# Optimization experiments

Measured on AMD Instinct MI355X. Metric: run time of the kernel, lower is better.

Reference implementation:

```python
import jax, jax.numpy as jnp
import numpy as np

DIM = 512
HEADS = 8
HEAD_DIM = DIM // HEADS
B, N = 4, 8192


def setup_inputs() -> dict:
    key = jax.random.key(0)
    k1, k2, k3, k4 = jax.random.split(key, 4)
    x = jax.random.normal(k1, (B, N, DIM), dtype=jnp.float32)
    # torch Linear weight is [out, in]; store transposed [in, out] for x @ W
    Wqkv = jax.random.normal(k2, (DIM, 3 * DIM), dtype=jnp.float32) * (DIM ** -0.5)
    Wout = jax.random.normal(k3, (DIM, DIM), dtype=jnp.float32) * (DIM ** -0.5)
    bout = jax.random.normal(k4, (DIM,), dtype=jnp.float32) * 0.01
    return {"x": x, "Wqkv": Wqkv, "Wout": Wout, "bout": bout}


def reference(x, Wqkv, Wout, bout):
    b, n, d = x.shape
    h, hd = HEADS, HEAD_DIM
    qkv = x @ Wqkv  # [b, n, 3d]
    q, k, v = jnp.split(qkv, 3, axis=-1)
    # [b, n, d] -> [b, h, n, hd]
    def to_heads(t):
        return t.reshape(b, n, h, hd).transpose(0, 2, 1, 3)
    q, k, v = to_heads(q), to_heads(k), to_heads(v)
    q = jax.nn.elu(q) + 1.0
    k = jax.nn.elu(k) + 1.0
    kv = jnp.einsum('bhnd,bhne->bhde', k, v)          # [b,h,hd,hd]
    z = 1.0 / (jnp.einsum('bhnd,bhd->bhn', q, k.sum(axis=2)) + 1e-6)
    out = jnp.einsum('bhnd,bhde->bhne', q, kv) * z[..., None]
    out = out.transpose(0, 2, 1, 3).reshape(b, n, d)
    # dropout in eval mode is identity
    return out @ Wout + bout
```

## Files before the change

### kernel.cpp

```cpp
#include <hip/hip_runtime.h>

typedef unsigned short u16;
typedef __bf16 bf16x8 __attribute__((ext_vector_type(8)));
typedef float f32x4 __attribute__((ext_vector_type(4)));

#define DEV static __device__ __forceinline__

DEV float bf2f(u16 u) { unsigned x = ((unsigned)u) << 16; return __builtin_bit_cast(float, x); }
DEV u16 f2bf(float f) {
  unsigned u = __builtin_bit_cast(unsigned, f);
  u += 0x7FFFu + ((u >> 16) & 1u);
  return (u16)(u >> 16);
}
DEV int swz(int b) { return b ^ ((((b >> 7) & 7)) << 4); }

#define GLD_LDS16(gp, lp)                                                    \
  __builtin_amdgcn_global_load_lds(                                          \
      (__attribute__((address_space(1))) void*)(void*)(gp),                  \
      (__attribute__((address_space(3))) void*)(lp), 16, 0, 0)

#define BAR() __builtin_amdgcn_s_barrier()
#define WAIT_LGKM0()                                                         \
  { asm volatile("s_waitcnt lgkmcnt(0)" ::: "memory");                       \
    __builtin_amdgcn_sched_barrier(0); }
#define WAIT_VM(n) asm volatile("s_waitcnt vmcnt(" #n ")" ::: "memory")

__global__ __launch_bounds__(256) void convert_bf16_kernel(
    const float* __restrict__ in, u16* __restrict__ out) {
  const size_t i = (size_t)blockIdx.x * 256 + threadIdx.x;
  const float4* p = (const float4*)in + 2 * i;
  float4 a = p[0], b = p[1];
  unsigned w0 = (unsigned)f2bf(a.x) | ((unsigned)f2bf(a.y) << 16);
  unsigned w1 = (unsigned)f2bf(a.z) | ((unsigned)f2bf(a.w) << 16);
  unsigned w2 = (unsigned)f2bf(b.x) | ((unsigned)f2bf(b.y) << 16);
  unsigned w3 = (unsigned)f2bf(b.z) | ((unsigned)f2bf(b.w) << 16);
  ((uint4*)out)[i] = make_uint4(w0, w1, w2, w3);
}

__global__ void transpose_bf16(const float* __restrict__ W, u16* __restrict__ Wt,
                               int K, int Ncols) {
  __shared__ float t[32][33];
  const int tx = threadIdx.x & 31, ty = threadIdx.x >> 5;
  const int n0 = blockIdx.x * 32, k0 = blockIdx.y * 32;
#pragma unroll
  for (int i = 0; i < 4; ++i)
    t[ty + i * 8][tx] = W[(size_t)(k0 + ty + i * 8) * Ncols + n0 + tx];
  __syncthreads();
#pragma unroll
  for (int i = 0; i < 4; ++i)
    Wt[(size_t)(n0 + ty + i * 8) * K + k0 + tx] = f2bf(t[tx][ty + i * 8]);
}

template <int MODE>
__global__ __launch_bounds__(512, 2) void gemm8_kernel(
    const u16* __restrict__ A, const u16* __restrict__ Bt,
    u16* __restrict__ qb, u16* __restrict__ kb, u16* __restrict__ vb,
    float* __restrict__ Cf, const float* __restrict__ bias) {
  constexpr int NX = (MODE == 0) ? 6 : 2;
  constexpr int K = 512;
  __shared__ __align__(16) u16 As[2][2][8192];
  __shared__ __align__(16) u16 Bs[2][2][8192];

  const int tid = threadIdx.x;
  const int lane = tid & 63;
  const int wid = tid >> 6;
  const int wr = wid >> 2;
  const int wcn = wid & 3;

  const int nwg = gridDim.x;
  const int pb = blockIdx.x;
  const int logical = (pb & 7) * (nwg >> 3) + (pb >> 3);
  const int rowBase = (logical / NX) * 256;
  const int colBase = (logical % NX) * 256;

  int soff[2], od[2];
#pragma unroll
  for (int i = 0; i < 2; ++i) {
    int o = (wid * 2 + i) * 1024 + lane * 16;
    int a = o ^ (((o >> 7) & 7) << 4);
    soff[i] = (a >> 7) * K + ((a & 127) >> 1);
    od[i] = (wid * 2 + i) * 512;
  }
  const u16* Abase = A + (size_t)rowBase * K;
  const u16* Bbase = Bt + (size_t)colBase * K;

#define STAGE_A(tau, h)                                                      \
  { const u16* g = Abase + (size_t)(h)*128 * K + (tau)*64;                   \
    _Pragma("unroll") for (int i = 0; i < 2; ++i)                            \
        GLD_LDS16(g + soff[i], &As[(tau)&1][h][od[i]]); }
#define STAGE_B(tau, h)                                                      \
  { const u16* g = Bbase + (size_t)(h)*128 * K + (tau)*64;                   \
    _Pragma("unroll") for (int i = 0; i < 2; ++i)                            \
        GLD_LDS16(g + soff[i], &Bs[(tau)&1][h][od[i]]); }

  const int sx = (lane & 7) << 4;
  int rb[2];
#pragma unroll
  for (int ks = 0; ks < 2; ++ks)
    rb[ks] = ((lane & 15) * 128 + ks * 64 + (lane >> 4) * 16) ^ sx;
  const char* Ahalf[2] = {(const char*)&As[0][wr][0], (const char*)&As[1][wr][0]};
  const char* Bhalf[2] = {(const char*)&Bs[0][wcn >> 1][0], (const char*)&Bs[1][wcn >> 1][0]};

  bf16x8 aA[4][2], bB0[2][2], bB1[2][2];
  f32x4 acc[8][4];
  f32x4 zv = {0.f, 0.f, 0.f, 0.f};
#pragma unroll
  for (int m = 0; m < 8; ++m)
#pragma unroll
    for (int n = 0; n < 4; ++n) acc[m][n] = zv;

#define LDA_FRAGS(par, mh)                                                   \
  _Pragma("unroll") for (int m = 0; m < 4; ++m)                              \
      _Pragma("unroll") for (int ks = 0; ks < 2; ++ks)                       \
          aA[m][ks] = *(const bf16x8*)(Ahalf[par] + (mh)*8192 + m * 2048 + rb[ks]);
#define LDB_FRAGS(par, nh, dst)                                              \
  _Pragma("unroll") for (int n = 0; n < 2; ++n)                              \
      _Pragma("unroll") for (int ks = 0; ks < 2; ++ks)                       \
          dst[n][ks] = *(const bf16x8*)(Bhalf[par] + (wcn & 1) * 8192 +      \
                                        (nh)*4096 + n * 2048 + rb[ks]);
#define MFMA_QUAD(mh, nh, bsrc)                                              \
  __builtin_amdgcn_s_setprio(1);                                             \
  _Pragma("unroll") for (int m = 0; m < 4; ++m)                              \
      _Pragma("unroll") for (int n = 0; n < 2; ++n)                          \
          _Pragma("unroll") for (int ks = 0; ks < 2; ++ks)                   \
              acc[(mh)*4 + m][(nh)*2 + n] =                                  \
                  __builtin_amdgcn_mfma_f32_16x16x32_bf16(                   \
                      aA[m][ks], bsrc[n][ks], acc[(mh)*4 + m][(nh)*2 + n],   \
                      0, 0, 0);                                              \
  __builtin_amdgcn_s_setprio(0);

  STAGE_A(0, 0); STAGE_A(0, 1); STAGE_B(0, 0); STAGE_B(0, 1);
  STAGE_B(1, 0); STAGE_A(1, 0);
  WAIT_VM(4);
  BAR();

  for (int t = 0; t < 6; t += 2) {
    LDA_FRAGS(0, 0); LDB_FRAGS(0, 0, bB0);
    STAGE_B(t + 1, 1);
    BAR(); WAIT_LGKM0();
    MFMA_QUAD(0, 0, bB0);
    BAR();
    LDB_FRAGS(0, 1, bB1);
    STAGE_A(t + 1, 1);
    BAR(); WAIT_LGKM0();
    MFMA_QUAD(0, 1, bB1);
    BAR();
    LDA_FRAGS(0, 1);
    STAGE_B(t + 2, 0);
    BAR(); WAIT_LGKM0();
    MFMA_QUAD(1, 1, bB1);
    BAR();
    STAGE_A(t + 2, 0);
    BAR(); WAIT_LGKM0();
    MFMA_QUAD(1, 0, bB0);
    WAIT_VM(4);
    BAR();
    LDA_FRAGS(1, 0); LDB_FRAGS(1, 0, bB0);
    STAGE_A(t + 2, 1);
    BAR(); WAIT_LGKM0();
    MFMA_QUAD(0, 0, bB0);
    BAR();
    LDB_FRAGS(1, 1, bB1);
    STAGE_B(t + 2, 1);
    BAR(); WAIT_LGKM0();
    MFMA_QUAD(0, 1, bB1);
    BAR();
    LDA_FRAGS(1, 1);
    STAGE_B(t + 3, 0);
    BAR(); WAIT_LGKM0();
    MFMA_QUAD(1, 1, bB1);
    BAR();
    STAGE_A(t + 3, 0);
    BAR(); WAIT_LGKM0();
    MFMA_QUAD(1, 0, bB0);
    WAIT_VM(4);
    BAR();
  }

  LDA_FRAGS(0, 0); LDB_FRAGS(0, 0, bB0);
  STAGE_B(7, 1);
  BAR(); WAIT_LGKM0();
  MFMA_QUAD(0, 0, bB0);
  BAR();
  LDB_FRAGS(0, 1, bB1);
  STAGE_A(7, 1);
  BAR(); WAIT_LGKM0();
  MFMA_QUAD(0, 1, bB1);
  BAR();
  LDA_FRAGS(0, 1);
  BAR(); WAIT_LGKM0();
  MFMA_QUAD(1, 1, bB1);
  BAR();
  BAR(); WAIT_LGKM0();
  MFMA_QUAD(1, 0, bB0);
  WAIT_VM(0);
  BAR();
  LDA_FRAGS(1, 0); LDB_FRAGS(1, 0, bB0);
  BAR(); WAIT_LGKM0();
  MFMA_QUAD(0, 0, bB0);
  BAR();
  LDB_FRAGS(1, 1, bB1);
  BAR(); WAIT_LGKM0();
  MFMA_QUAD(0, 1, bB1);
  BAR();
  LDA_FRAGS(1, 1);
  BAR(); WAIT_LGKM0();
  MFMA_QUAD(1, 1, bB1);
  BAR();
  BAR(); WAIT_LGKM0();
  MFMA_QUAD(1, 0, bB0);

  if (MODE == 0) {
    u16* dst = (colBase < 512) ? qb : (colBase < 1024) ? kb : vb;
    const int cb2 = colBase & 511;
    const bool doelu = (colBase < 1024);
    const int rbBase = (rowBase >> 4) + wr * 8;
    const int cbBase = (cb2 >> 4) + wcn * 4;
#pragma unroll
    for (int mi = 0; mi < 8; ++mi) {
#pragma unroll
      for (int ni = 0; ni < 4; ++ni) {
        float v[4];
#pragma unroll
        for (int r = 0; r < 4; ++r) {
          float t2 = acc[mi][ni][r];
          v[r] = doelu ? ((t2 > 0.f) ? t2 + 1.f : __expf(t2)) : t2;
        }
        unsigned lo = (unsigned)f2bf(v[0]) | ((unsigned)f2bf(v[1]) << 16);
        unsigned hi = (unsigned)f2bf(v[2]) | ((unsigned)f2bf(v[3]) << 16);
        size_t base = (((size_t)(rbBase + mi) * 32 + (cbBase + ni)) * 64 + lane) * 4;
        *(uint2*)(dst + base) = make_uint2(lo, hi);
      }
    }
  } else {
#pragma unroll
    for (int mi = 0; mi < 8; ++mi) {
#pragma unroll
      for (int ni = 0; ni < 4; ++ni) {
        const int col = colBase + wcn * 64 + ni * 16 + (lane & 15);
#pragma unroll
        for (int r = 0; r < 4; ++r) {
          const int row = rowBase + wr * 128 + mi * 16 + (lane >> 4) * 4 + r;
          Cf[(size_t)row * 512 + col] = acc[mi][ni][r] + bias[col];
        }
      }
    }
  }
#undef STAGE_A
#undef STAGE_B
#undef LDA_FRAGS
#undef LDB_FRAGS
#undef MFMA_QUAD
}

__global__ __launch_bounds__(256, 2) void kv_partial_mfma(
    const u16* __restrict__ kb, const u16* __restrict__ vb,
    float* __restrict__ part) {
  __shared__ __align__(16) char lds[81920];
  const int tid = threadIdx.x, lane = tid & 63, wid = tid >> 6;
  const int chunk = blockIdx.x;
  const int bh = blockIdx.y;
  const int b = bh >> 3, h = bh & 7;
  const int hcb = h * 4;

  char* kTc = lds + wid * 16384;
  char* vTc = kTc + 8192;
  const int rb0 = b * 512 + chunk * 64 + wid * 16;

  uint4 kreg[8], vreg[8];

#define KV_LOAD(it)                                                          \
  _Pragma("unroll") for (int q = 0; q < 8; ++q) {                            \
    int u = q * 64 + lane;                                                   \
    int fid = u >> 5, w = u & 31;                                            \
    int rbl = fid >> 2, cbi = fid & 3;                                       \
    size_t fb = ((size_t)(rb0 + (it)*4 + rbl) * 32 + hcb + cbi) * 32 + w;    \
    kreg[q] = ((const uint4*)kb)[fb];                                        \
    vreg[q] = ((const uint4*)vb)[fb];                                        \
  }

#define KV_WRITE()                                                           \
  _Pragma("unroll") for (int q = 0; q < 8; ++q) {                            \
    int u = q * 64 + lane;                                                   \
    int fid = u >> 5, w = u & 31;                                            \
    int rbl = fid >> 2, cbi = fid & 3;                                       \
    int l0 = 2 * w;                                                          \
    int d0 = cbi * 16 + (l0 & 15);                                           \
    int n0 = rbl * 16 + (l0 >> 4) * 4;                                       \
    int a0 = swz(d0 * 128 + n0 * 2);                                         \
    int a1 = swz((d0 + 1) * 128 + n0 * 2);                                   \
    *(uint2*)(kTc + a0) = make_uint2(kreg[q].x, kreg[q].y);                  \
    *(uint2*)(kTc + a1) = make_uint2(kreg[q].z, kreg[q].w);                  \
    *(uint2*)(vTc + a0) = make_uint2(vreg[q].x, vreg[q].y);                  \
    *(uint2*)(vTc + a1) = make_uint2(vreg[q].z, vreg[q].w);                  \
  }

  const uint4 onesu = make_uint4(0x3F803F80u, 0x3F803F80u, 0x3F803F80u, 0x3F803F80u);
  const bf16x8 ones = __builtin_bit_cast(bf16x8, onesu);

  f32x4 zv = {0.f, 0.f, 0.f, 0.f};
  f32x4 acc[4][5];
#pragma unroll
  for (int mb = 0; mb < 4; ++mb)
#pragma unroll
    for (int eb = 0; eb < 5; ++eb) acc[mb][eb] = zv;

  KV_LOAD(0);
#pragma unroll
  for (int it = 0; it < 4; ++it) {
    WAIT_VM(0);
    KV_WRITE();
    if (it < 3) KV_LOAD(it + 1);
    WAIT_LGKM0();
#pragma unroll
    for (int ks = 0; ks < 2; ++ks) {
      bf16x8 afr[4], bvf[4];
#pragma unroll
      for (int mb = 0; mb < 4; ++mb)
        afr[mb] = *(const bf16x8*)(kTc + swz((mb * 16 + (lane & 15)) * 128 +
                                             (ks * 32 + (lane >> 4) * 8) * 2));
#pragma unroll
      for (int eb = 0; eb < 4; ++eb)
        bvf[eb] = *(const bf16x8*)(vTc + swz((eb * 16 + (lane & 15)) * 128 +
                                             (ks * 32 + (lane >> 4) * 8) * 2));
      WAIT_LGKM0();
#pragma unroll
      for (int mb = 0; mb < 4; ++mb) {
#pragma unroll
        for (int eb = 0; eb < 4; ++eb)
          acc[mb][eb] = __builtin_amdgcn_mfma_f32_16x16x32_bf16(
              afr[mb], bvf[eb], acc[mb][eb], 0, 0, 0);
        acc[mb][4] = __builtin_amdgcn_mfma_f32_16x16x32_bf16(
            afr[mb], ones, acc[mb][4], 0, 0, 0);
      }
    }
  }

  __syncthreads();
  float* red = (float*)lds;
#pragma unroll
  for (int mb = 0; mb < 4; ++mb)
#pragma unroll
    for (int eb = 0; eb < 5; ++eb)
      ((f32x4*)red)[wid * 1280 + (mb * 5 + eb) * 64 + lane] = acc[mb][eb];
  __syncthreads();

  float* pp = part + ((size_t)bh * 8 + chunk) * 5120;
  const int lane_s = tid >> 2, r = tid & 3;
#pragma unroll
  for (int fi = 0; fi < 20; ++fi) {
    float s = red[fi * 256 + tid] + red[5120 + fi * 256 + tid] +
              red[10240 + fi * 256 + tid] + red[15360 + fi * 256 + tid];
    const int mb = fi / 5, eb = fi % 5;
    const int d = mb * 16 + (lane_s >> 4) * 4 + r;
    if (eb < 4) {
      pp[d * 80 + eb * 16 + (lane_s & 15)] = s;
    } else if ((lane_s & 15) == 0) {
      pp[d * 80 + 64] = s;
    }
  }
#undef KV_LOAD
#undef KV_WRITE
}

__global__ void kv_reduce_kernel(const float* __restrict__ part,
                                 float* __restrict__ kv_ext) {
  const int idx = blockIdx.x * 256 + threadIdx.x;
  const int bh = idx / 5120;
  const int de = idx % 5120;
  const int e = de % 80;
  float s = 0.f;
  if (e <= 64) {
    for (int c = 0; c < 8; ++c) s += part[((size_t)bh * 8 + c) * 5120 + de];
  }
  kv_ext[idx] = s;
}

__global__ __launch_bounds__(256, 2) void attn_kernel(
    const u16* __restrict__ qb, const float* __restrict__ kv_ext,
    u16* __restrict__ attn) {
  __shared__ __align__(16) float kvs[64 * 80];
  __shared__ __align__(16) u16 qs[4][64 * 64];
  const int tid = threadIdx.x, lane = tid & 63, wid = tid >> 6;
  const int nchunk = blockIdx.x, bh = blockIdx.y;
  const int b = bh >> 3, h = bh & 7;

#pragma unroll
  for (int i = 0; i < 20; ++i)
    kvs[i * 256 + tid] = kv_ext[(size_t)bh * 5120 + i * 256 + tid];
  __syncthreads();

  bf16x8 bfr[5][2];
#pragma unroll
  for (int eb = 0; eb < 5; ++eb)
#pragma unroll
    for (int ksi = 0; ksi < 2; ++ksi) {
      unsigned pw[4];
#pragma unroll
      for (int jj = 0; jj < 4; ++jj) {
        int d0 = ksi * 32 + (lane >> 4) * 8 + 2 * jj;
        int e = eb * 16 + (lane & 15);
        unsigned lo = f2bf(kvs[d0 * 80 + e]);
        unsigned hi = f2bf(kvs[(d0 + 1) * 80 + e]);
        pw[jj] = lo | (hi << 16);
      }
      uint4 u = make_uint4(pw[0], pw[1], pw[2], pw[3]);
      bfr[eb][ksi] = __builtin_bit_cast(bf16x8, u);
    }

  const size_t row0 = (size_t)b * 8192 + (size_t)nchunk * 256 + wid * 64;
  const int rbQ = (int)(row0 >> 4);
  const int hcbQ = h * 4;
  char* qsw = (char*)&qs[wid][0];
#pragma unroll
  for (int it = 0; it < 8; ++it) {
    int flat = it * 64 + lane;
    int frag = flat >> 5, w = flat & 31;
    int rb_i = frag >> 2, cb_i = frag & 3;
    size_t src = (((size_t)(rbQ + rb_i) * 32 + hcbQ + cb_i) * 64 + w * 2) * 4;
    uint4 q4 = *(const uint4*)(qb + src);
    int l0 = w * 2;
    int row = rb_i * 16 + ((l0 >> 4) << 2);
    int col = cb_i * 16 + (l0 & 15);
    int bb = row * 128 + col * 2;
    *(unsigned*)(qsw + swz(bb)) = (q4.x & 0xFFFF) | ((q4.z & 0xFFFF) << 16);
    *(unsigned*)(qsw + swz(bb + 128)) = (q4.x >> 16) | (q4.z & 0xFFFF0000u);
    *(unsigned*)(qsw + swz(bb + 256)) = (q4.y & 0xFFFF) | ((q4.w & 0xFFFF) << 16);
    *(unsigned*)(qsw + swz(bb + 384)) = (q4.y >> 16) | (q4.w & 0xFFFF0000u);
  }
  WAIT_LGKM0();

  f32x4 zv = {0.f, 0.f, 0.f, 0.f};
  f32x4 acc[4][5];
#pragma unroll
  for (int m = 0; m < 4; ++m)
#pragma unroll
    for (int eb = 0; eb < 5; ++eb) acc[m][eb] = zv;

#pragma unroll
  for (int m = 0; m < 4; ++m)
#pragma unroll
    for (int ksi = 0; ksi < 2; ++ksi) {
      int bb = (m * 16 + (lane & 15)) * 128 + (ksi * 32 + (lane >> 4) * 8) * 2;
      bf16x8 af = *(const bf16x8*)(qsw + swz(bb));
#pragma unroll
      for (int eb = 0; eb < 5; ++eb)
        acc[m][eb] = __builtin_amdgcn_mfma_f32_16x16x32_bf16(af, bfr[eb][ksi], acc[m][eb], 0, 0, 0);
    }

#pragma unroll
  for (int m = 0; m < 4; ++m) {
#pragma unroll
    for (int r = 0; r < 4; ++r) {
      float den = __shfl(acc[m][4][r], lane & ~15, 64);
      float zr = 1.f / (den + 1e-6f);
      int row = m * 16 + (lane >> 4) * 4 + r;
#pragma unroll
      for (int eb = 0; eb < 4; ++eb) {
        int col = eb * 16 + (lane & 15);
        *(u16*)(qsw + swz(row * 128 + col * 2)) = f2bf(acc[m][eb][r] * zr);
      }
    }
  }
  WAIT_LGKM0();
#pragma unroll
  for (int jt = 0; jt < 8; ++jt) {
    int flat = jt * 64 + lane;
    int row = flat >> 3, w = flat & 7;
    uint4 val = *(const uint4*)(qsw + swz(row * 128 + w * 16));
    *(uint4*)(attn + (row0 + row) * 512 + h * 64 + w * 8) = val;
  }
}

extern "C" void kernel_launch(void* const* d_in, const int* in_sizes, int n_in,
                              void* d_out, int out_size, void* d_ws, size_t ws_size,
                              hipStream_t stream) {
  const float* x = (const float*)d_in[0];
  const float* Wqkv = (const float*)d_in[1];
  const float* Wout = (const float*)d_in[2];
  const float* bout = (const float*)d_in[3];
  float* out = (float*)d_out;

  char* ws = (char*)d_ws;
  u16* qb = (u16*)ws;        ws += (size_t)32768 * 512 * 2;
  u16* kb = (u16*)ws;        ws += (size_t)32768 * 512 * 2;
  u16* vb = (u16*)ws;        ws += (size_t)32768 * 512 * 2;
  u16* wqkv_t = (u16*)ws;    ws += (size_t)1536 * 512 * 2;
  u16* wout_t = (u16*)ws;    ws += (size_t)512 * 512 * 2;
  float* kv_ext = (float*)ws; ws += (size_t)32 * 64 * 80 * 4;
  float* part = (float*)ws;   ws += (size_t)32 * 8 * 64 * 80 * 4;

  u16* xb = (u16*)d_out;

  convert_bf16_kernel<<<8192, 256, 0, stream>>>(x, xb);
  transpose_bf16<<<dim3(1536 / 32, 512 / 32), 256, 0, stream>>>(Wqkv, wqkv_t, 512, 1536);
  transpose_bf16<<<dim3(512 / 32, 512 / 32), 256, 0, stream>>>(Wout, wout_t, 512, 512);
  gemm8_kernel<0><<<768, 512, 0, stream>>>(xb, wqkv_t, qb, kb, vb, nullptr, nullptr);
  kv_partial_mfma<<<dim3(8, 32), 256, 0, stream>>>(kb, vb, part);
  kv_reduce_kernel<<<640, 256, 0, stream>>>(part, kv_ext);
  attn_kernel<<<dim3(32, 32), 256, 0, stream>>>(qb, kv_ext, vb);
  gemm8_kernel<1><<<256, 512, 0, stream>>>(vb, wout_t, nullptr, nullptr, nullptr, out, bout);
}
```

Before: 144.5 us.

## Make QKV GEMM persistent over three output tiles per workgroup

The QKV projection GEMM now launches 256 workgroups, each covering three consecutive 256x256 output tiles rather than one. The K-loop runs across all three tiles, so staging of the next tile's A/B slices overlaps the current tile's MFMAs, and the per-tile epilogue runs inside the loop before the accumulators are reset. This removes the per-tile pipeline prologue and drain and the launch of 768 separate workgroups. The tile order changes so consecutive tiles step along rows within a column panel. On a 256-CU part this gives one workgroup per CU, which may reduce latency hiding and leaves the mid-loop epilogue exposed while the prefetched loads are in flight.

```diff
diff --git a/kernel.cpp b/kernel.cpp
--- a/kernel.cpp
+++ b/kernel.cpp
@@ -56,7 +56,8 @@
     const u16* __restrict__ A, const u16* __restrict__ Bt,
     u16* __restrict__ qb, u16* __restrict__ kb, u16* __restrict__ vb,
     float* __restrict__ Cf, const float* __restrict__ bias) {
-  constexpr int NX = (MODE == 0) ? 6 : 2;
+  constexpr int PANELS = (MODE == 0) ? 3 : 1;
+  constexpr int NT = 8 * PANELS;
   constexpr int K = 512;
   __shared__ __align__(16) u16 As[2][2][8192];
   __shared__ __align__(16) u16 Bs[2][2][8192];
@@ -70,8 +71,7 @@
   const int nwg = gridDim.x;
   const int pb = blockIdx.x;
   const int logical = (pb & 7) * (nwg >> 3) + (pb >> 3);
-  const int rowBase = (logical / NX) * 256;
-  const int colBase = (logical % NX) * 256;
+  const int T0 = logical * PANELS;
 
   int soff[2], od[2];
 #pragma unroll
@@ -81,17 +81,17 @@
     soff[i] = (a >> 7) * K + ((a & 127) >> 1);
     od[i] = (wid * 2 + i) * 512;
   }
-  const u16* Abase = A + (size_t)rowBase * K;
-  const u16* Bbase = Bt + (size_t)colBase * K;
-
-#define STAGE_A(tau, h)                                                      \
-  { const u16* g = Abase + (size_t)(h)*128 * K + (tau)*64;                   \
+
+#define STAGE_A(s, h)                                                        \
+  { int _T = T0 + ((s) >> 3);                                                \
+    const u16* g = A + (size_t)((_T & 127) * 256 + (h)*128) * K + ((s)&7) * 64; \
     _Pragma("unroll") for (int i = 0; i < 2; ++i)                            \
-        GLD_LDS16(g + soff[i], &As[(tau)&1][h][od[i]]); }
-#define STAGE_B(tau, h)                                                      \
-  { const u16* g = Bbase + (size_t)(h)*128 * K + (tau)*64;                   \
+        GLD_LDS16(g + soff[i], &As[(s)&1][h][od[i]]); }
+#define STAGE_B(s, h)                                                        \
+  { int _T = T0 + ((s) >> 3);                                                \
+    const u16* g = Bt + (size_t)((_T >> 7) * 256 + (h)*128) * K + ((s)&7) * 64; \
     _Pragma("unroll") for (int i = 0; i < 2; ++i)                            \
-        GLD_LDS16(g + soff[i], &Bs[(tau)&1][h][od[i]]); }
+        GLD_LDS16(g + soff[i], &Bs[(s)&1][h][od[i]]); }
 
   const int sx = (lane & 7) << 4;
   int rb[2];
@@ -129,12 +129,51 @@
                       0, 0, 0);                                              \
   __builtin_amdgcn_s_setprio(0);
 
+#define EPILOGUE(pp)                                                         \
+  { const int _Te = T0 + (pp);                                               \
+    const int rowB = (_Te & 127) * 256, colB = (_Te >> 7) * 256;             \
+    if (MODE == 0) {                                                         \
+      u16* dst = (colB < 512) ? qb : (colB < 1024) ? kb : vb;                \
+      const int cb2 = colB & 511;                                            \
+      const bool doelu = (colB < 1024);                                      \
+      const int rbB = (rowB >> 4) + wr * 8;                                  \
+      const int cbB = (cb2 >> 4) + wcn * 4;                                  \
+      _Pragma("unroll") for (int mi = 0; mi < 8; ++mi) {                     \
+        _Pragma("unroll") for (int ni = 0; ni < 4; ++ni) {                   \
+          float v[4];                                                        \
+          _Pragma("unroll") for (int r = 0; r < 4; ++r) {                    \
+            float t2 = acc[mi][ni][r];                                       \
+            v[r] = doelu ? ((t2 > 0.f) ? t2 + 1.f : __expf(t2)) : t2;        \
+          }                                                                  \
+          unsigned lo = (unsigned)f2bf(v[0]) | ((unsigned)f2bf(v[1]) << 16); \
+          unsigned hi = (unsigned)f2bf(v[2]) | ((unsigned)f2bf(v[3]) << 16); \
+          size_t base = (((size_t)(rbB + mi) * 32 + (cbB + ni)) * 64 + lane) * 4; \
+          *(uint2*)(dst + base) = make_uint2(lo, hi);                        \
+        }                                                                    \
+      }                                                                      \
+    } else {                                                                 \
+      _Pragma("unroll") for (int mi = 0; mi < 8; ++mi) {                     \
+        _Pragma("unroll") for (int ni = 0; ni < 4; ++ni) {                   \
+          const int col = colB + wcn * 64 + ni * 16 + (lane & 15);           \
+          _Pragma("unroll") for (int r = 0; r < 4; ++r) {                    \
+            const int row = rowB + wr * 128 + mi * 16 + (lane >> 4) * 4 + r; \
+            Cf[(size_t)row * 512 + col] = acc[mi][ni][r] + bias[col];        \
+          }                                                                  \
+        }                                                                    \
+      }                                                                      \
+    }                                                                        \
+  }
+#define ZERO_ACC()                                                           \
+  _Pragma("unroll") for (int m = 0; m < 8; ++m)                              \
+      _Pragma("unroll") for (int n = 0; n < 4; ++n) acc[m][n] = zv;
+
   STAGE_A(0, 0); STAGE_A(0, 1); STAGE_B(0, 0); STAGE_B(0, 1);
   STAGE_B(1, 0); STAGE_A(1, 0);
   WAIT_VM(4);
   BAR();
 
-  for (int t = 0; t < 6; t += 2) {
+#pragma unroll 1
+  for (int t = 0; t < NT - 2; t += 2) {
     LDA_FRAGS(0, 0); LDB_FRAGS(0, 0, bB0);
     STAGE_B(t + 1, 1);
     BAR(); WAIT_LGKM0();
@@ -175,15 +214,19 @@
     MFMA_QUAD(1, 0, bB0);
     WAIT_VM(4);
     BAR();
+    if (PANELS > 1 && (t & 7) == 6) {
+      EPILOGUE((t + 1) >> 3);
+      ZERO_ACC();
+    }
   }
 
   LDA_FRAGS(0, 0); LDB_FRAGS(0, 0, bB0);
-  STAGE_B(7, 1);
+  STAGE_B(NT - 1, 1);
   BAR(); WAIT_LGKM0();
   MFMA_QUAD(0, 0, bB0);
   BAR();
   LDB_FRAGS(0, 1, bB1);
-  STAGE_A(7, 1);
+  STAGE_A(NT - 1, 1);
   BAR(); WAIT_LGKM0();
   MFMA_QUAD(0, 1, bB1);
   BAR();
@@ -210,47 +253,15 @@
   BAR(); WAIT_LGKM0();
   MFMA_QUAD(1, 0, bB0);
 
-  if (MODE == 0) {
-    u16* dst = (colBase < 512) ? qb : (colBase < 1024) ? kb : vb;
-    const int cb2 = colBase & 511;
-    const bool doelu = (colBase < 1024);
-    const int rbBase = (rowBase >> 4) + wr * 8;
-    const int cbBase = (cb2 >> 4) + wcn * 4;
-#pragma unroll
-    for (int mi = 0; mi < 8; ++mi) {
-#pragma unroll
-      for (int ni = 0; ni < 4; ++ni) {
-        float v[4];
-#pragma unroll
-        for (int r = 0; r < 4; ++r) {
-          float t2 = acc[mi][ni][r];
-          v[r] = doelu ? ((t2 > 0.f) ? t2 + 1.f : __expf(t2)) : t2;
-        }
-        unsigned lo = (unsigned)f2bf(v[0]) | ((unsigned)f2bf(v[1]) << 16);
-        unsigned hi = (unsigned)f2bf(v[2]) | ((unsigned)f2bf(v[3]) << 16);
-        size_t base = (((size_t)(rbBase + mi) * 32 + (cbBase + ni)) * 64 + lane) * 4;
-        *(uint2*)(dst + base) = make_uint2(lo, hi);
-      }
-    }
-  } else {
-#pragma unroll
-    for (int mi = 0; mi < 8; ++mi) {
-#pragma unroll
-      for (int ni = 0; ni < 4; ++ni) {
-        const int col = colBase + wcn * 64 + ni * 16 + (lane & 15);
-#pragma unroll
-        for (int r = 0; r < 4; ++r) {
-          const int row = rowBase + wr * 128 + mi * 16 + (lane >> 4) * 4 + r;
-          Cf[(size_t)row * 512 + col] = acc[mi][ni][r] + bias[col];
-        }
-      }
-    }
-  }
+  EPILOGUE(PANELS - 1);
+
 #undef STAGE_A
 #undef STAGE_B
 #undef LDA_FRAGS
 #undef LDB_FRAGS
 #undef MFMA_QUAD
+#undef EPILOGUE
+#undef ZERO_ACC
 }
 
 __global__ __launch_bounds__(256, 2) void kv_partial_mfma(
@@ -495,7 +506,7 @@
   convert_bf16_kernel<<<8192, 256, 0, stream>>>(x, xb);
   transpose_bf16<<<dim3(1536 / 32, 512 / 32), 256, 0, stream>>>(Wqkv, wqkv_t, 512, 1536);
   transpose_bf16<<<dim3(512 / 32, 512 / 32), 256, 0, stream>>>(Wout, wout_t, 512, 512);
-  gemm8_kernel<0><<<768, 512, 0, stream>>>(xb, wqkv_t, qb, kb, vb, nullptr, nullptr);
+  gemm8_kernel<0><<<256, 512, 0, stream>>>(xb, wqkv_t, qb, kb, vb, nullptr, nullptr);
   kv_partial_mfma<<<dim3(8, 32), 256, 0, stream>>>(kb, vb, part);
   kv_reduce_kernel<<<640, 256, 0, stream>>>(part, kv_ext);
   attn_kernel<<<dim3(32, 32), 256, 0, stream>>>(qb, kv_ext, vb);
```

Measured after the change: 156.5 us. 1.08x slower.

## Fuse fp32-to-bf16 conversion of x into QKV GEMM A-tile loading

Applied to the files above, without the earlier changes.

Removes the separate conversion kernel and has the QKV GEMM load fp32 x directly into registers. It then converts the values with v_cvt_pk_bf16_f32 and writes them to LDS, with the issue and write steps interleaved into the existing pipeline. This drops one kernel launch and the write and re-read of a bf16 copy of x. In exchange the GEMM reads twice the bytes for A, uses extra registers, and replaces direct global-to-LDS loads with register staging and new vmcnt waits.

```diff
diff --git a/kernel.cpp b/kernel.cpp
--- a/kernel.cpp
+++ b/kernel.cpp
@@ -12,6 +12,11 @@
   u += 0x7FFFu + ((u >> 16) & 1u);
   return (u16)(u >> 16);
 }
+DEV unsigned cvtpk(float lo, float hi) {
+  unsigned r;
+  asm("v_cvt_pk_bf16_f32 %0, %1, %2" : "=v"(r) : "v"(lo), "v"(hi));
+  return r;
+}
 DEV int swz(int b) { return b ^ ((((b >> 7) & 7)) << 4); }
 
 #define GLD_LDS16(gp, lp)                                                    \
@@ -25,18 +30,6 @@
     __builtin_amdgcn_sched_barrier(0); }
 #define WAIT_VM(n) asm volatile("s_waitcnt vmcnt(" #n ")" ::: "memory")
 
-__global__ __launch_bounds__(256) void convert_bf16_kernel(
-    const float* __restrict__ in, u16* __restrict__ out) {
-  const size_t i = (size_t)blockIdx.x * 256 + threadIdx.x;
-  const float4* p = (const float4*)in + 2 * i;
-  float4 a = p[0], b = p[1];
-  unsigned w0 = (unsigned)f2bf(a.x) | ((unsigned)f2bf(a.y) << 16);
-  unsigned w1 = (unsigned)f2bf(a.z) | ((unsigned)f2bf(a.w) << 16);
-  unsigned w2 = (unsigned)f2bf(b.x) | ((unsigned)f2bf(b.y) << 16);
-  unsigned w3 = (unsigned)f2bf(b.z) | ((unsigned)f2bf(b.w) << 16);
-  ((uint4*)out)[i] = make_uint4(w0, w1, w2, w3);
-}
-
 __global__ void transpose_bf16(const float* __restrict__ W, u16* __restrict__ Wt,
                                int K, int Ncols) {
   __shared__ float t[32][33];
@@ -53,7 +46,7 @@
 
 template <int MODE>
 __global__ __launch_bounds__(512, 2) void gemm8_kernel(
-    const u16* __restrict__ A, const u16* __restrict__ Bt,
+    const void* __restrict__ Av, const u16* __restrict__ Bt,
     u16* __restrict__ qb, u16* __restrict__ kb, u16* __restrict__ vb,
     float* __restrict__ Cf, const float* __restrict__ bias) {
   constexpr int NX = (MODE == 0) ? 6 : 2;
@@ -73,6 +66,9 @@
   const int rowBase = (logical / NX) * 256;
   const int colBase = (logical % NX) * 256;
 
+  const float* Axf = (const float*)Av;
+  const u16* Axb = (const u16*)Av;
+
   int soff[2], od[2];
 #pragma unroll
   for (int i = 0; i < 2; ++i) {
@@ -81,17 +77,32 @@
     soff[i] = (a >> 7) * K + ((a & 127) >> 1);
     od[i] = (wid * 2 + i) * 512;
   }
-  const u16* Abase = A + (size_t)rowBase * K;
+  const u16* Abase = Axb + (size_t)rowBase * K;
   const u16* Bbase = Bt + (size_t)colBase * K;
 
+#define STAGE_B(tau, h)                                                      \
+  { const u16* g = Bbase + (size_t)(h)*128 * K + (tau)*64;                   \
+    _Pragma("unroll") for (int i = 0; i < 2; ++i)                            \
+        GLD_LDS16(g + soff[i], &Bs[(tau)&1][h][od[i]]); }
 #define STAGE_A(tau, h)                                                      \
   { const u16* g = Abase + (size_t)(h)*128 * K + (tau)*64;                   \
     _Pragma("unroll") for (int i = 0; i < 2; ++i)                            \
         GLD_LDS16(g + soff[i], &As[(tau)&1][h][od[i]]); }
-#define STAGE_B(tau, h)                                                      \
-  { const u16* g = Bbase + (size_t)(h)*128 * K + (tau)*64;                   \
-    _Pragma("unroll") for (int i = 0; i < 2; ++i)                            \
-        GLD_LDS16(g + soff[i], &Bs[(tau)&1][h][od[i]]); }
+#define ISSUE_A(R, tau, h)                                                   \
+  { const float* g = Axf + (size_t)(rowBase + (h)*128) * K + (tau)*64;       \
+    _Pragma("unroll") for (int i = 0; i < 2; ++i) {                          \
+      R[2 * i] = *(const float4*)(g + soff[i]);                              \
+      R[2 * i + 1] = *(const float4*)(g + soff[i] + 4);                      \
+    } }
+#define WRITE_A(R, tau, h)                                                   \
+  { _Pragma("unroll") for (int i = 0; i < 2; ++i) {                          \
+      uint4 w;                                                               \
+      w.x = cvtpk(R[2 * i].x, R[2 * i].y);                                   \
+      w.y = cvtpk(R[2 * i].z, R[2 * i].w);                                   \
+      w.z = cvtpk(R[2 * i + 1].x, R[2 * i + 1].y);                           \
+      w.w = cvtpk(R[2 * i + 1].z, R[2 * i + 1].w);                           \
+      *(uint4*)&As[(tau)&1][h][od[i] + lane * 8] = w;                        \
+    } }
 
   const int sx = (lane & 7) << 4;
   int rb[2];
@@ -102,6 +113,7 @@
   const char* Bhalf[2] = {(const char*)&Bs[0][wcn >> 1][0], (const char*)&Bs[1][wcn >> 1][0]};
 
   bf16x8 aA[4][2], bB0[2][2], bB1[2][2];
+  float4 aR0[4], aR1[4];
   f32x4 acc[8][4];
   f32x4 zv = {0.f, 0.f, 0.f, 0.f};
 #pragma unroll
@@ -129,34 +141,52 @@
                       0, 0, 0);                                              \
   __builtin_amdgcn_s_setprio(0);
 
-  STAGE_A(0, 0); STAGE_A(0, 1); STAGE_B(0, 0); STAGE_B(0, 1);
-  STAGE_B(1, 0); STAGE_A(1, 0);
-  WAIT_VM(4);
-  BAR();
-
+  if constexpr (MODE == 0) {
+    ISSUE_A(aR0, 0, 0); ISSUE_A(aR1, 0, 1);
+    STAGE_B(0, 0); STAGE_B(0, 1);
+    WAIT_VM(8); WRITE_A(aR0, 0, 0);
+    WAIT_VM(4); WRITE_A(aR1, 0, 1);
+    ISSUE_A(aR0, 1, 0);
+    WAIT_VM(0); WRITE_A(aR0, 1, 0);
+    ISSUE_A(aR1, 1, 1); STAGE_B(1, 0);
+    WAIT_LGKM0();
+    BAR();
+  } else {
+    STAGE_A(0, 0); STAGE_A(0, 1); STAGE_B(0, 0); STAGE_B(0, 1);
+    STAGE_B(1, 0); STAGE_A(1, 0);
+    WAIT_VM(4);
+    BAR();
+  }
+
+#pragma unroll 1
   for (int t = 0; t < 6; t += 2) {
     LDA_FRAGS(0, 0); LDB_FRAGS(0, 0, bB0);
+    if constexpr (MODE == 0) { ISSUE_A(aR0, t + 2, 0); }
     STAGE_B(t + 1, 1);
     BAR(); WAIT_LGKM0();
     MFMA_QUAD(0, 0, bB0);
     BAR();
     LDB_FRAGS(0, 1, bB1);
-    STAGE_A(t + 1, 1);
+    if constexpr (MODE == 0) { WAIT_VM(8); WRITE_A(aR1, t + 1, 1); }
+    else { STAGE_A(t + 1, 1); }
     BAR(); WAIT_LGKM0();
     MFMA_QUAD(0, 1, bB1);
     BAR();
     LDA_FRAGS(0, 1);
+    if constexpr (MODE == 0) { ISSUE_A(aR1, t + 2, 1); }
     STAGE_B(t + 2, 0);
     BAR(); WAIT_LGKM0();
     MFMA_QUAD(1, 1, bB1);
     BAR();
-    STAGE_A(t + 2, 0);
+    if constexpr (MODE == 0) { WAIT_VM(6); WRITE_A(aR0, t + 2, 0); }
+    else { STAGE_A(t + 2, 0); }
     BAR(); WAIT_LGKM0();
     MFMA_QUAD(1, 0, bB0);
-    WAIT_VM(4);
+    if constexpr (MODE == 1) WAIT_VM(4);
     BAR();
     LDA_FRAGS(1, 0); LDB_FRAGS(1, 0, bB0);
-    STAGE_A(t + 2, 1);
+    if constexpr (MODE == 0) { ISSUE_A(aR0, t + 3, 0); WAIT_VM(6); WRITE_A(aR1, t + 2, 1); }
+    else { STAGE_A(t + 2, 1); }
     BAR(); WAIT_LGKM0();
     MFMA_QUAD(0, 0, bB0);
     BAR();
@@ -166,14 +196,16 @@
     MFMA_QUAD(0, 1, bB1);
     BAR();
     LDA_FRAGS(1, 1);
+    if constexpr (MODE == 0) { ISSUE_A(aR1, t + 3, 1); }
     STAGE_B(t + 3, 0);
     BAR(); WAIT_LGKM0();
     MFMA_QUAD(1, 1, bB1);
     BAR();
-    STAGE_A(t + 3, 0);
+    if constexpr (MODE == 0) { WAIT_VM(6); WRITE_A(aR0, t + 3, 0); }
+    else { STAGE_A(t + 3, 0); }
     BAR(); WAIT_LGKM0();
     MFMA_QUAD(1, 0, bB0);
-    WAIT_VM(4);
+    if constexpr (MODE == 1) WAIT_VM(4);
     BAR();
   }
 
@@ -183,7 +215,8 @@
   MFMA_QUAD(0, 0, bB0);
   BAR();
   LDB_FRAGS(0, 1, bB1);
-  STAGE_A(7, 1);
+  if constexpr (MODE == 0) { WAIT_VM(4); WRITE_A(aR1, 7, 1); }
+  else { STAGE_A(7, 1); }
   BAR(); WAIT_LGKM0();
   MFMA_QUAD(0, 1, bB1);
   BAR();
@@ -248,6 +281,8 @@
   }
 #undef STAGE_A
 #undef STAGE_B
+#undef ISSUE_A
+#undef WRITE_A
 #undef LDA_FRAGS
 #undef LDB_FRAGS
 #undef MFMA_QUAD
@@ -490,12 +525,9 @@
   float* kv_ext = (float*)ws; ws += (size_t)32 * 64 * 80 * 4;
   float* part = (float*)ws;   ws += (size_t)32 * 8 * 64 * 80 * 4;
 
-  u16* xb = (u16*)d_out;
-
-  convert_bf16_kernel<<<8192, 256, 0, stream>>>(x, xb);
   transpose_bf16<<<dim3(1536 / 32, 512 / 32), 256, 0, stream>>>(Wqkv, wqkv_t, 512, 1536);
   transpose_bf16<<<dim3(512 / 32, 512 / 32), 256, 0, stream>>>(Wout, wout_t, 512, 512);
-  gemm8_kernel<0><<<768, 512, 0, stream>>>(xb, wqkv_t, qb, kb, vb, nullptr, nullptr);
+  gemm8_kernel<0><<<768, 512, 0, stream>>>(x, wqkv_t, qb, kb, vb, nullptr, nullptr);
   kv_partial_mfma<<<dim3(8, 32), 256, 0, stream>>>(kb, vb, part);
   kv_reduce_kernel<<<640, 256, 0, stream>>>(part, kv_ext);
   attn_kernel<<<dim3(32, 32), 256, 0, stream>>>(qb, kv_ext, vb);
```

Measured after the change: 150.7 us. 1.04x slower.

## Fuse attention output computation into the output projection GEMM

Applied to the files above, without the earlier changes.

Removes the separate attn_kernel and generates the A operand of the output GEMM on the fly: each K-tile (one head) is computed from q fragments and the per-head kv matrix with MFMAs, normalized, and written directly into the swizzled LDS A buffer. The kv reduction now also pre-packs kv into bf16 MFMA fragment layout so the fused kernel can load it directly. This drops the global round-trip of the attention output and one launch. In exchange, the GEMM main loop has extra per-tile MFMA and LDS work plus more register pressure.

```diff
diff --git a/kernel.cpp b/kernel.cpp
--- a/kernel.cpp
+++ b/kernel.cpp
@@ -51,12 +51,10 @@
     Wt[(size_t)(n0 + ty + i * 8) * K + k0 + tx] = f2bf(t[tx][ty + i * 8]);
 }
 
-template <int MODE>
-__global__ __launch_bounds__(512, 2) void gemm8_kernel(
+__global__ __launch_bounds__(512, 2) void gemm_qkv_kernel(
     const u16* __restrict__ A, const u16* __restrict__ Bt,
-    u16* __restrict__ qb, u16* __restrict__ kb, u16* __restrict__ vb,
-    float* __restrict__ Cf, const float* __restrict__ bias) {
-  constexpr int NX = (MODE == 0) ? 6 : 2;
+    u16* __restrict__ qb, u16* __restrict__ kb, u16* __restrict__ vb) {
+  constexpr int NX = 6;
   constexpr int K = 512;
   __shared__ __align__(16) u16 As[2][2][8192];
   __shared__ __align__(16) u16 Bs[2][2][8192];
@@ -64,8 +62,7 @@
   const int tid = threadIdx.x;
   const int lane = tid & 63;
   const int wid = tid >> 6;
-  const int wr = wid >> 2;
-  const int wcn = wid & 3;
+  const int wr = wid >> 2, wcn = wid & 3;
 
   const int nwg = gridDim.x;
   const int pb = blockIdx.x;
@@ -210,7 +207,7 @@
   BAR(); WAIT_LGKM0();
   MFMA_QUAD(1, 0, bB0);
 
-  if (MODE == 0) {
+  {
     u16* dst = (colBase < 512) ? qb : (colBase < 1024) ? kb : vb;
     const int cb2 = colBase & 511;
     const bool doelu = (colBase < 1024);
@@ -230,19 +227,6 @@
         unsigned hi = (unsigned)f2bf(v[2]) | ((unsigned)f2bf(v[3]) << 16);
         size_t base = (((size_t)(rbBase + mi) * 32 + (cbBase + ni)) * 64 + lane) * 4;
         *(uint2*)(dst + base) = make_uint2(lo, hi);
-      }
-    }
-  } else {
-#pragma unroll
-    for (int mi = 0; mi < 8; ++mi) {
-#pragma unroll
-      for (int ni = 0; ni < 4; ++ni) {
-        const int col = colBase + wcn * 64 + ni * 16 + (lane & 15);
-#pragma unroll
-        for (int r = 0; r < 4; ++r) {
-          const int row = rowBase + wr * 128 + mi * 16 + (lane >> 4) * 4 + r;
-          Cf[(size_t)row * 512 + col] = acc[mi][ni][r] + bias[col];
-        }
       }
     }
   }
@@ -363,113 +347,212 @@
 #undef KV_WRITE
 }
 
-__global__ void kv_reduce_kernel(const float* __restrict__ part,
-                                 float* __restrict__ kv_ext) {
-  const int idx = blockIdx.x * 256 + threadIdx.x;
-  const int bh = idx / 5120;
-  const int de = idx % 5120;
-  const int e = de % 80;
-  float s = 0.f;
-  if (e <= 64) {
-    for (int c = 0; c < 8; ++c) s += part[((size_t)bh * 8 + c) * 5120 + de];
-  }
-  kv_ext[idx] = s;
-}
-
-__global__ __launch_bounds__(256, 2) void attn_kernel(
-    const u16* __restrict__ qb, const float* __restrict__ kv_ext,
-    u16* __restrict__ attn) {
-  __shared__ __align__(16) float kvs[64 * 80];
-  __shared__ __align__(16) u16 qs[4][64 * 64];
-  const int tid = threadIdx.x, lane = tid & 63, wid = tid >> 6;
-  const int nchunk = blockIdx.x, bh = blockIdx.y;
-  const int b = bh >> 3, h = bh & 7;
-
-#pragma unroll
-  for (int i = 0; i < 20; ++i)
-    kvs[i * 256 + tid] = kv_ext[(size_t)bh * 5120 + i * 256 + tid];
+__global__ __launch_bounds__(256) void kv_reduce_frag(
+    const float* __restrict__ part, uint4* __restrict__ kvf) {
+  __shared__ float kvs[5120];
+  const int tid = threadIdx.x;
+  const int bh = blockIdx.x;
+#pragma unroll
+  for (int i = 0; i < 20; ++i) {
+    int idx = i * 256 + tid;
+    float s = 0.f;
+    if (idx % 80 <= 64) {
+      for (int c = 0; c < 8; ++c) s += part[((size_t)bh * 8 + c) * 5120 + idx];
+    }
+    kvs[idx] = s;
+  }
   __syncthreads();
 
-  bf16x8 bfr[5][2];
-#pragma unroll
-  for (int eb = 0; eb < 5; ++eb)
-#pragma unroll
-    for (int ksi = 0; ksi < 2; ++ksi) {
+  const int lane = tid & 63, f = tid >> 6;
+#pragma unroll
+  for (int i = 0; i < 3; ++i) {
+    int combo = i * 4 + f;
+    if (combo < 10) {
+      int eb = combo >> 1, ks = combo & 1;
       unsigned pw[4];
 #pragma unroll
       for (int jj = 0; jj < 4; ++jj) {
-        int d0 = ksi * 32 + (lane >> 4) * 8 + 2 * jj;
+        int d0 = ks * 32 + (lane >> 4) * 8 + 2 * jj;
         int e = eb * 16 + (lane & 15);
         unsigned lo = f2bf(kvs[d0 * 80 + e]);
         unsigned hi = f2bf(kvs[(d0 + 1) * 80 + e]);
         pw[jj] = lo | (hi << 16);
       }
-      uint4 u = make_uint4(pw[0], pw[1], pw[2], pw[3]);
-      bfr[eb][ksi] = __builtin_bit_cast(bf16x8, u);
+      kvf[(size_t)bh * 640 + combo * 64 + lane] = make_uint4(pw[0], pw[1], pw[2], pw[3]);
     }
-
-  const size_t row0 = (size_t)b * 8192 + (size_t)nchunk * 256 + wid * 64;
-  const int rbQ = (int)(row0 >> 4);
-  const int hcbQ = h * 4;
-  char* qsw = (char*)&qs[wid][0];
-#pragma unroll
-  for (int it = 0; it < 8; ++it) {
-    int flat = it * 64 + lane;
-    int frag = flat >> 5, w = flat & 31;
-    int rb_i = frag >> 2, cb_i = frag & 3;
-    size_t src = (((size_t)(rbQ + rb_i) * 32 + hcbQ + cb_i) * 64 + w * 2) * 4;
-    uint4 q4 = *(const uint4*)(qb + src);
-    int l0 = w * 2;
-    int row = rb_i * 16 + ((l0 >> 4) << 2);
-    int col = cb_i * 16 + (l0 & 15);
-    int bb = row * 128 + col * 2;
-    *(unsigned*)(qsw + swz(bb)) = (q4.x & 0xFFFF) | ((q4.z & 0xFFFF) << 16);
-    *(unsigned*)(qsw + swz(bb + 128)) = (q4.x >> 16) | (q4.z & 0xFFFF0000u);
-    *(unsigned*)(qsw + swz(bb + 256)) = (q4.y & 0xFFFF) | ((q4.w & 0xFFFF) << 16);
-    *(unsigned*)(qsw + swz(bb + 384)) = (q4.y >> 16) | (q4.w & 0xFFFF0000u);
-  }
+  }
+}
+
+__global__ __launch_bounds__(512, 2) void gemm1f_kernel(
+    const u16* __restrict__ qb, const uint4* __restrict__ kvf,
+    const u16* __restrict__ Bt, float* __restrict__ Cf,
+    const float* __restrict__ bias) {
+  constexpr int K = 512;
+  __shared__ __align__(16) u16 As[2][2][8192];
+  __shared__ __align__(16) u16 Bs[2][2][8192];
+  __shared__ __align__(16) u16 qstage[8][1024];
+
+  const int tid = threadIdx.x, lane = tid & 63, wid = tid >> 6;
+  const int wr = wid >> 2, wcn = wid & 3;
+  const int nwg = gridDim.x, pb = blockIdx.x;
+  const int logical = (pb & 7) * (nwg >> 3) + (pb >> 3);
+  const int rowBase = (logical >> 1) * 256;
+  const int colBase = (logical & 1) * 256;
+  const int bIdx = rowBase >> 13;
+
+  int soff[2], od[2];
+#pragma unroll
+  for (int i = 0; i < 2; ++i) {
+    int o = (wid * 2 + i) * 1024 + lane * 16;
+    int a = o ^ (((o >> 7) & 7) << 4);
+    soff[i] = (a >> 7) * K + ((a & 127) >> 1);
+    od[i] = (wid * 2 + i) * 512;
+  }
+  const u16* Bbase = Bt + (size_t)colBase * K;
+
+#define STAGE_BF(tau)                                                        \
+  { _Pragma("unroll") for (int h = 0; h < 2; ++h) {                          \
+      const u16* g = Bbase + (size_t)h * 128 * K + (tau)*64;                 \
+      _Pragma("unroll") for (int i = 0; i < 2; ++i)                          \
+          GLD_LDS16(g + soff[i], &Bs[(tau)&1][h][od[i]]); } }
+
+  const int sx = (lane & 7) << 4;
+  int rb[2];
+#pragma unroll
+  for (int ks = 0; ks < 2; ++ks)
+    rb[ks] = ((lane & 15) * 128 + ks * 64 + (lane >> 4) * 16) ^ sx;
+  const char* AhalfBase = (const char*)&As[0][wr][0];
+  const char* BhalfBase = (const char*)&Bs[0][wcn >> 1][0];
+  char* qsw = (char*)&qstage[wid][0];
+  char* adstBase = (char*)&As[0][wid >> 2][0];
+
+  const int rbQ = (rowBase + wid * 32) >> 4;
+  const size_t kvfBase = (size_t)bIdx * 8 * 640;
+
+  bf16x8 aA[4][2], bB0[2][2], bB1[2][2], bfrv[5][2];
+  uint4 qreg[4];
+  f32x4 acc[8][4], acc2[2][5];
+  f32x4 zv = {0.f, 0.f, 0.f, 0.f};
+#pragma unroll
+  for (int m = 0; m < 8; ++m)
+#pragma unroll
+    for (int n = 0; n < 4; ++n) acc[m][n] = zv;
+
+#define QLOAD(tt)                                                            \
+  _Pragma("unroll") for (int qi = 0; qi < 4; ++qi) {                         \
+    int u = qi * 64 + lane, fid = u >> 5, w = u & 31;                        \
+    int rb_i = fid >> 2, cbi = fid & 3;                                      \
+    qreg[qi] = ((const uint4*)qb)[((size_t)(rbQ + rb_i) * 32 + (tt)*4 + cbi) * 32 + w]; \
+  }
+#define BFRLOAD(tt)                                                          \
+  _Pragma("unroll") for (int eb = 0; eb < 5; ++eb)                           \
+      _Pragma("unroll") for (int ks = 0; ks < 2; ++ks)                       \
+          bfrv[eb][ks] = __builtin_bit_cast(bf16x8,                          \
+              kvf[kvfBase + (tt)*640 + (eb * 2 + ks) * 64 + lane]);
+
+#define AGEN(tt)                                                             \
+  { _Pragma("unroll") for (int sp = 0; sp < 2; ++sp) {                       \
+      _Pragma("unroll") for (int eb = 0; eb < 5; ++eb) acc2[sp][eb] = zv;    \
+      _Pragma("unroll") for (int j = 0; j < 2; ++j) {                        \
+        uint4 q4 = qreg[sp * 2 + j];                                         \
+        int u = (sp * 2 + j) * 64 + lane, fid = u >> 5, w = u & 31;          \
+        int cbi = fid & 3, l0 = 2 * w;                                       \
+        int row0 = (l0 >> 4) << 2, col0 = cbi * 16 + (l0 & 15);              \
+        int bb = row0 * 128 + col0 * 2;                                      \
+        *(unsigned*)(qsw + swz(bb)) = (q4.x & 0xFFFFu) | ((q4.z & 0xFFFFu) << 16); \
+        *(unsigned*)(qsw + swz(bb + 128)) = (q4.x >> 16) | (q4.z & 0xFFFF0000u); \
+        *(unsigned*)(qsw + swz(bb + 256)) = (q4.y & 0xFFFFu) | ((q4.w & 0xFFFFu) << 16); \
+        *(unsigned*)(qsw + swz(bb + 384)) = (q4.y >> 16) | (q4.w & 0xFFFF0000u); \
+      }                                                                      \
+      WAIT_LGKM0();                                                          \
+      bf16x8 af0 = *(const bf16x8*)(qsw + rb[0]);                            \
+      bf16x8 af1 = *(const bf16x8*)(qsw + rb[1]);                            \
+      WAIT_LGKM0();                                                          \
+      _Pragma("unroll") for (int eb = 0; eb < 5; ++eb) {                     \
+        acc2[sp][eb] = __builtin_amdgcn_mfma_f32_16x16x32_bf16(              \
+            af0, bfrv[eb][0], acc2[sp][eb], 0, 0, 0);                        \
+        acc2[sp][eb] = __builtin_amdgcn_mfma_f32_16x16x32_bf16(              \
+            af1, bfrv[eb][1], acc2[sp][eb], 0, 0, 0);                        \
+      }                                                                      \
+    }                                                                        \
+    char* adst = adstBase + ((tt)&1) * 32768;                                \
+    _Pragma("unroll") for (int m = 0; m < 2; ++m)                            \
+        _Pragma("unroll") for (int r = 0; r < 4; ++r) {                      \
+          float den = __shfl(acc2[m][4][r], lane & ~15, 64);                 \
+          float zr = 1.f / (den + 1e-6f);                                    \
+          int lrow = (wid & 3) * 32 + m * 16 + (lane >> 4) * 4 + r;          \
+          _Pragma("unroll") for (int eb = 0; eb < 4; ++eb) {                 \
+            int col = eb * 16 + (lane & 15);                                 \
+            *(u16*)(adst + swz(lrow * 128 + col * 2)) = f2bf(acc2[m][eb][r] * zr); \
+          }                                                                  \
+        } }
+
+#define LDA_FRAGS(Ah, mh)                                                    \
+  _Pragma("unroll") for (int m = 0; m < 4; ++m)                              \
+      _Pragma("unroll") for (int ks = 0; ks < 2; ++ks)                       \
+          aA[m][ks] = *(const bf16x8*)((Ah) + (mh)*8192 + m * 2048 + rb[ks]);
+#define LDB_FRAGS(Bh, nh, dst)                                               \
+  _Pragma("unroll") for (int n = 0; n < 2; ++n)                              \
+      _Pragma("unroll") for (int ks = 0; ks < 2; ++ks)                       \
+          dst[n][ks] = *(const bf16x8*)((Bh) + (wcn & 1) * 8192 +            \
+                                        (nh)*4096 + n * 2048 + rb[ks]);
+#define MFMA_QUAD(mh, nh, bsrc)                                              \
+  __builtin_amdgcn_s_setprio(1);                                             \
+  _Pragma("unroll") for (int m = 0; m < 4; ++m)                              \
+      _Pragma("unroll") for (int n = 0; n < 2; ++n)                          \
+          _Pragma("unroll") for (int ks = 0; ks < 2; ++ks)                   \
+              acc[(mh)*4 + m][(nh)*2 + n] =                                  \
+                  __builtin_amdgcn_mfma_f32_16x16x32_bf16(                   \
+                      aA[m][ks], bsrc[n][ks], acc[(mh)*4 + m][(nh)*2 + n],   \
+                      0, 0, 0);                                              \
+  __builtin_amdgcn_s_setprio(0);
+
+  QLOAD(0); BFRLOAD(0); STAGE_BF(0); STAGE_BF(1);
+  AGEN(0);
+  WAIT_VM(0);
   WAIT_LGKM0();
-
-  f32x4 zv = {0.f, 0.f, 0.f, 0.f};
-  f32x4 acc[4][5];
-#pragma unroll
-  for (int m = 0; m < 4; ++m)
-#pragma unroll
-    for (int eb = 0; eb < 5; ++eb) acc[m][eb] = zv;
-
-#pragma unroll
-  for (int m = 0; m < 4; ++m)
-#pragma unroll
-    for (int ksi = 0; ksi < 2; ++ksi) {
-      int bb = (m * 16 + (lane & 15)) * 128 + (ksi * 32 + (lane >> 4) * 8) * 2;
-      bf16x8 af = *(const bf16x8*)(qsw + swz(bb));
-#pragma unroll
-      for (int eb = 0; eb < 5; ++eb)
-        acc[m][eb] = __builtin_amdgcn_mfma_f32_16x16x32_bf16(af, bfr[eb][ksi], acc[m][eb], 0, 0, 0);
-    }
-
-#pragma unroll
-  for (int m = 0; m < 4; ++m) {
-#pragma unroll
-    for (int r = 0; r < 4; ++r) {
-      float den = __shfl(acc[m][4][r], lane & ~15, 64);
-      float zr = 1.f / (den + 1e-6f);
-      int row = m * 16 + (lane >> 4) * 4 + r;
-#pragma unroll
-      for (int eb = 0; eb < 4; ++eb) {
-        int col = eb * 16 + (lane & 15);
-        *(u16*)(qsw + swz(row * 128 + col * 2)) = f2bf(acc[m][eb][r] * zr);
+  BAR();
+
+#pragma unroll 1
+  for (int tau = 0; tau < 8; ++tau) {
+    const char* Ah = AhalfBase + (tau & 1) * 32768;
+    const char* Bh = BhalfBase + (tau & 1) * 32768;
+    LDA_FRAGS(Ah, 0); LDB_FRAGS(Bh, 0, bB0); LDB_FRAGS(Bh, 1, bB1);
+    if (tau < 7) QLOAD(tau + 1);
+    WAIT_LGKM0();
+    MFMA_QUAD(0, 0, bB0);
+    MFMA_QUAD(0, 1, bB1);
+    LDA_FRAGS(Ah, 1);
+    WAIT_LGKM0();
+    MFMA_QUAD(1, 1, bB1);
+    MFMA_QUAD(1, 0, bB0);
+    BAR();
+    if (tau < 7) BFRLOAD(tau + 1);
+    if (tau < 6) STAGE_BF(tau + 2);
+    if (tau < 7) AGEN(tau + 1);
+    WAIT_LGKM0();
+    BAR();
+  }
+
+#pragma unroll
+  for (int mi = 0; mi < 8; ++mi) {
+#pragma unroll
+    for (int ni = 0; ni < 4; ++ni) {
+      const int col = colBase + wcn * 64 + ni * 16 + (lane & 15);
+#pragma unroll
+      for (int r = 0; r < 4; ++r) {
+        const int row = rowBase + wr * 128 + mi * 16 + (lane >> 4) * 4 + r;
+        Cf[(size_t)row * 512 + col] = acc[mi][ni][r] + bias[col];
       }
     }
   }
-  WAIT_LGKM0();
-#pragma unroll
-  for (int jt = 0; jt < 8; ++jt) {
-    int flat = jt * 64 + lane;
-    int row = flat >> 3, w = flat & 7;
-    uint4 val = *(const uint4*)(qsw + swz(row * 128 + w * 16));
-    *(uint4*)(attn + (row0 + row) * 512 + h * 64 + w * 8) = val;
-  }
+#undef STAGE_BF
+#undef QLOAD
+#undef BFRLOAD
+#undef AGEN
+#undef LDA_FRAGS
+#undef LDB_FRAGS
+#undef MFMA_QUAD
 }
 
 extern "C" void kernel_launch(void* const* d_in, const int* in_sizes, int n_in,
@@ -487,17 +570,16 @@
   u16* vb = (u16*)ws;        ws += (size_t)32768 * 512 * 2;
   u16* wqkv_t = (u16*)ws;    ws += (size_t)1536 * 512 * 2;
   u16* wout_t = (u16*)ws;    ws += (size_t)512 * 512 * 2;
-  float* kv_ext = (float*)ws; ws += (size_t)32 * 64 * 80 * 4;
-  float* part = (float*)ws;   ws += (size_t)32 * 8 * 64 * 80 * 4;
+  uint4* kvf = (uint4*)ws;   ws += (size_t)32 * 640 * 16;
+  float* part = (float*)ws;  ws += (size_t)32 * 8 * 64 * 80 * 4;
 
   u16* xb = (u16*)d_out;
 
   convert_bf16_kernel<<<8192, 256, 0, stream>>>(x, xb);
   transpose_bf16<<<dim3(1536 / 32, 512 / 32), 256, 0, stream>>>(Wqkv, wqkv_t, 512, 1536);
   transpose_bf16<<<dim3(512 / 32, 512 / 32), 256, 0, stream>>>(Wout, wout_t, 512, 512);
-  gemm8_kernel<0><<<768, 512, 0, stream>>>(xb, wqkv_t, qb, kb, vb, nullptr, nullptr);
+  gemm_qkv_kernel<<<768, 512, 0, stream>>>(xb, wqkv_t, qb, kb, vb);
   kv_partial_mfma<<<dim3(8, 32), 256, 0, stream>>>(kb, vb, part);
-  kv_reduce_kernel<<<640, 256, 0, stream>>>(part, kv_ext);
-  attn_kernel<<<dim3(32, 32), 256, 0, stream>>>(qb, kv_ext, vb);
-  gemm8_kernel<1><<<256, 512, 0, stream>>>(vb, wout_t, nullptr, nullptr, nullptr, out, bout);
-}
+  kv_reduce_frag<<<32, 256, 0, stream>>>(part, kvf);
+  gemm1f_kernel<<<256, 512, 0, stream>>>(qb, kvf, wout_t, out, bout);
+}
```

Measured after the change: 230.0 us. 1.59x slower.
